# Kernel tuning notes

Hardware: AMD Instinct MI355X
Metric: run time of the kernel (lower is better)

## Reference

```python
import jax, jax.numpy as jnp
import numpy as np

B, S, D = 8, 2048, 256
H = 4
DH = D // H  # 64


def setup_inputs() -> dict:
    key = jax.random.key(0)
    ks = jax.random.split(key, 6)
    x = jax.random.normal(ks[0], (B, S, D), dtype=jnp.float32)
    # Linear weights stored as (d_in, d_out) so y = x @ W (+ b)
    scale = 1.0 / np.sqrt(D)
    w_q = jax.random.normal(ks[1], (D, D), dtype=jnp.float32) * scale
    w_k = jax.random.normal(ks[2], (D, D), dtype=jnp.float32) * scale
    w_v = jax.random.normal(ks[3], (D, D), dtype=jnp.float32) * scale
    w_o = jax.random.normal(ks[4], (D, D), dtype=jnp.float32) * scale
    b_o = jax.random.normal(ks[5], (D,), dtype=jnp.float32) * 0.01
    return {"x": x, "w_q": w_q, "w_k": w_k, "w_v": w_v, "w_o": w_o, "b_o": b_o}


def reference(x, w_q, w_k, w_v, w_o, b_o):
    b, s, _ = x.shape
    # project and split heads: [b, h, s, dh]
    q = (x @ w_q).reshape(b, s, H, DH).transpose(0, 2, 1, 3)
    k = (x @ w_k).reshape(b, s, H, DH).transpose(0, 2, 1, 3)
    v = (x @ w_v).reshape(b, s, H, DH).transpose(0, 2, 1, 3)
    # full attention matrix [b, h, s, s] (matches original non-fused math)
    scores = jnp.einsum('bhqd,bhkd->bhqk', q, k) / jnp.sqrt(jnp.float32(DH))
    attn = jax.nn.softmax(scores, axis=-1)  # dropout is identity in eval
    ctx = jnp.einsum('bhqk,bhkd->bhqd', attn, v)
    ctx = ctx.transpose(0, 2, 1, 3).reshape(b, s, H * DH)
    return ctx @ w_o + b_o
```

## Files before the change

kernel.cpp:

```cpp
#include <hip/hip_runtime.h>
#include <hip/hip_fp16.h>
#include <math.h>

typedef _Float16 f16;
typedef _Float16 f16x8 __attribute__((ext_vector_type(8)));
typedef float f32x4 __attribute__((ext_vector_type(4)));
typedef float f32x16 __attribute__((ext_vector_type(16)));
typedef unsigned int u32;
typedef unsigned int u32x4 __attribute__((ext_vector_type(4)));

#define BB 8
#define SS 2048
#define DD 256
#define HH 4
#define DHH 64

#define LOG2E 1.44269504088896340736f
#define MOFF2 (4.0f * LOG2E)
#define QSCALE (0.125f * LOG2E)

static __device__ __forceinline__ u32 pkrtz(float a, float b) {
  auto t = __builtin_amdgcn_cvt_pkrtz(a, b);
  return __builtin_bit_cast(u32, t);
}

__global__ __launch_bounds__(256) void prep_kernel(
    const float* __restrict__ wq, const float* __restrict__ wk,
    const float* __restrict__ wv, const float* __restrict__ wo,
    f16* __restrict__ wqkvT, f16* __restrict__ woT) {
  __shared__ f16 lds[64][72];
  int dout0 = blockIdx.x * 64;
  int k0 = blockIdx.y * 64;
  const float* src;
  f16* dst;
  int col0, drow;
  if (dout0 < 256)      { src = wq; dst = wqkvT; col0 = dout0;       drow = dout0; }
  else if (dout0 < 512) { src = wk; dst = wqkvT; col0 = dout0 - 256; drow = dout0; }
  else if (dout0 < 768) { src = wv; dst = wqkvT; col0 = dout0 - 512; drow = dout0; }
  else                  { src = wo; dst = woT;   col0 = dout0 - 768; drow = dout0 - 768; }

  int dl = threadIdx.x & 63, kl = threadIdx.x >> 6;
#pragma unroll
  for (int i = 0; i < 16; i++) {
    int kloc = i * 4 + kl;
    lds[kloc][dl] = (f16)src[(size_t)(k0 + kloc) * 256 + col0 + dl];
  }
  __syncthreads();
  int row_l = threadIdx.x >> 2, kq = threadIdx.x & 3;
  f16x8 v0, v1;
#pragma unroll
  for (int j = 0; j < 8; j++) v0[j] = lds[kq * 16 + j][row_l];
#pragma unroll
  for (int j = 0; j < 8; j++) v1[j] = lds[kq * 16 + 8 + j][row_l];
  f16* p = dst + (size_t)(drow + row_l) * 256 + k0 + kq * 16;
  *(f16x8*)p = v0;
  *(f16x8*)(p + 8) = v1;
}

__global__ __launch_bounds__(256) void qkv_gemm(
    const float* __restrict__ x, const f16* __restrict__ wT,
    f16* __restrict__ Q, f16* __restrict__ K, f16* __restrict__ VT) {
  __shared__ __attribute__((aligned(16))) f16 astage[8][4][64][8];
  __shared__ __attribute__((aligned(16))) f16 bstage[8][4][64][8];
  __shared__ __attribute__((aligned(16))) f16 lds_t[64][72];
  int m0 = blockIdx.x * 64;
  int wave = threadIdx.x >> 6, lane = threadIdx.x & 63;
  int lm = lane & 15, quad = lane >> 4;
  int bb = m0 >> 11, s0 = m0 & 2047;

  {
    int row = threadIdx.x >> 2;
    int c0 = (threadIdx.x & 3) * 64;
    const float* xr = x + (size_t)(m0 + row) * 256 + c0;
#pragma unroll
    for (int i = 0; i < 8; i++) {
      f32x4 lo = *(const f32x4*)(xr + i * 8);
      f32x4 hi = *(const f32x4*)(xr + i * 8 + 4);
      f16x8 v;
#pragma unroll
      for (int j = 0; j < 4; j++) { v[j] = (f16)lo[j]; v[j + 4] = (f16)hi[j]; }
      int col = c0 + i * 8;
      *(f16x8*)&astage[col >> 5][row >> 4][((col >> 3) & 3) * 16 + (row & 15)][0] = v;
    }
  }
  __syncthreads();
  f16x8 a[8];
#pragma unroll
  for (int kk = 0; kk < 8; kk++) a[kk] = *(const f16x8*)&astage[kk][wave][lane][0];

  f16x8 breg[8];
  auto bload = [&](int n0) {
#pragma unroll
    for (int kk = 0; kk < 8; kk++)
      breg[kk] = *(const f16x8*)(wT + (size_t)(n0 + wave * 16 + lm) * 256 + kk * 32 + quad * 8);
  };
  bload(0);

  for (int i = 0; i < 12; i++) {
#pragma unroll
    for (int kk = 0; kk < 8; kk++)
      *(f16x8*)&bstage[kk][wave][lane][0] = breg[kk];
    __syncthreads();
    if (i + 1 < 12) bload((i + 1) * 64);

    f32x4 acc[4] = {};
#pragma unroll
    for (int kk = 0; kk < 8; kk++)
#pragma unroll
      for (int nt = 0; nt < 4; nt++) {
        f16x8 b = *(const f16x8*)&bstage[kk][nt][lane][0];
        acc[nt] = __builtin_amdgcn_mfma_f32_16x16x32_f16(a[kk], b, acc[nt], 0, 0, 0);
      }

    int h = i & 3;
    if (i < 8) {
      float qsc = (i < 4) ? QSCALE : 1.0f;
#pragma unroll
      for (int nt = 0; nt < 4; nt++)
#pragma unroll
        for (int r = 0; r < 4; r++)
          lds_t[wave * 16 + quad * 4 + r][nt * 16 + lm] = (f16)(acc[nt][r] * qsc);
      __syncthreads();
      int rr = threadIdx.x >> 2, cc = threadIdx.x & 3;
      f16* dst = ((i < 4) ? Q : K) +
                 (((size_t)(bb * HH + h) * SS + s0 + rr) << 6) + cc * 16;
      *(f16x8*)dst = *(const f16x8*)&lds_t[rr][cc * 16];
      *(f16x8*)(dst + 8) = *(const f16x8*)&lds_t[rr][cc * 16 + 8];
    } else {
#pragma unroll
      for (int nt = 0; nt < 4; nt++)
#pragma unroll
        for (int r = 0; r < 4; r++)
          lds_t[nt * 16 + lm][wave * 16 + quad * 4 + r] = (f16)acc[nt][r];
      __syncthreads();
      int rr = threadIdx.x >> 2, cc = threadIdx.x & 3;
      f16* vrow = VT + ((size_t)(bb * HH + h) * DHH + rr) * SS + s0;
      *(f16x8*)(vrow + cc * 16) = *(const f16x8*)&lds_t[rr][cc * 16];
      *(f16x8*)(vrow + cc * 16 + 8) = *(const f16x8*)&lds_t[rr][cc * 16 + 8];
    }
    __syncthreads();
  }
}

__global__ __launch_bounds__(512, 2) void attn_kernel(
    const f16* __restrict__ Q, const f16* __restrict__ K,
    const f16* __restrict__ VT, f16* __restrict__ ctx) {
  __shared__ __attribute__((aligned(16))) f16 kv[2][2][2][8][64][8];

  int qb = blockIdx.x, hd = blockIdx.y, b = blockIdx.z;
  int w = threadIdx.x >> 6, lane = threadIdx.x & 63;
  int half = w >> 2, wl = w & 3;
  int l31 = lane & 31, hi = lane >> 5, hi8 = hi * 8;
  const f16* Qbh = Q + (size_t)(b * HH + hd) * SS * DHH;
  const f16* Kbh = K + (size_t)(b * HH + hd) * SS * DHH;
  const f16* Vbh = VT + (size_t)(b * HH + hd) * DHH * SS;
  int q0 = qb * 128 + wl * 32;
  int kh0 = half * 1024;

  f16x8 tk0, tk1, tv0, tv1;
  auto stage_load = [&](int key0) {
    tk0 = *(const f16x8*)(Kbh + (size_t)(key0 + l31) * DHH + wl * 16 + hi8);
    tk1 = *(const f16x8*)(Kbh + (size_t)(key0 + 32 + l31) * DHH + wl * 16 + hi8);
    tv0 = *(const f16x8*)(Vbh + (size_t)l31 * SS + key0 + wl * 16 + hi8);
    tv1 = *(const f16x8*)(Vbh + (size_t)(32 + l31) * SS + key0 + wl * 16 + hi8);
  };
  auto stage_write = [&](int buf) {
    *(f16x8*)&kv[half][buf][0][wl][lane][0] = tk0;
    *(f16x8*)&kv[half][buf][0][4 + wl][lane][0] = tk1;
    *(f16x8*)&kv[half][buf][1][wl][lane][0] = tv0;
    *(f16x8*)&kv[half][buf][1][4 + wl][lane][0] = tv1;
  };

  f16x8 aq[4];
  {
    const f16* qrow = Qbh + (size_t)(q0 + l31) * DHH + hi8;
#pragma unroll
    for (int kp = 0; kp < 4; kp++) aq[kp] = *(const f16x8*)(qrow + kp * 16);
  }
  f16x8 vones;
#pragma unroll
  for (int j = 0; j < 8; j++) vones[j] = (f16)1.0f;
  f32x16 minit;
#pragma unroll
  for (int r = 0; r < 16; r++) minit[r] = -MOFF2;

  f32x16 accO0, accO1, accL;
#pragma unroll
  for (int r = 0; r < 16; r++) { accO0[r] = 0.f; accO1[r] = 0.f; accL[r] = 0.f; }

  stage_load(kh0);
  stage_write(0);
  stage_load(kh0 + 64);

  const int NT = 1024 / 64;
  for (int t = 0; t < NT; t++) {
    int cur = t & 1;
    __syncthreads();

    if (t + 1 < NT) {
      stage_write(cur ^ 1);
      if (t + 2 < NT) stage_load(kh0 + (t + 2) * 64);
    }

    f32x16 accST[2];
#pragma unroll
    for (int kp = 0; kp < 4; kp++)
#pragma unroll
      for (int nt = 0; nt < 2; nt++) {
        f16x8 kf = *(const f16x8*)&kv[half][cur][0][nt * 4 + kp][lane][0];
        accST[nt] = __builtin_amdgcn_mfma_f32_32x32x16_f16(
            kf, aq[kp], kp == 0 ? minit : accST[nt], 0, 0, 0);
      }

    f16x8 pa[4];
#pragma unroll
    for (int nt = 0; nt < 2; nt++) {
      u32 u[4][2];
#pragma unroll
      for (int bq = 0; bq < 4; bq++) {
        float p0 = __builtin_amdgcn_exp2f(accST[nt][4 * bq + 0]);
        float p1 = __builtin_amdgcn_exp2f(accST[nt][4 * bq + 1]);
        float p2 = __builtin_amdgcn_exp2f(accST[nt][4 * bq + 2]);
        float p3 = __builtin_amdgcn_exp2f(accST[nt][4 * bq + 3]);
        u[bq][0] = pkrtz(p0, p1);
        u[bq][1] = pkrtz(p2, p3);
      }
#pragma unroll
      for (int sl = 0; sl < 2; sl++) {
        auto r0 = __builtin_amdgcn_permlane32_swap(u[2 * sl][0], u[2 * sl + 1][0],
                                                   false, false);
        auto r1 = __builtin_amdgcn_permlane32_swap(u[2 * sl][1], u[2 * sl + 1][1],
                                                   false, false);
        u32x4 wv = {(u32)r0[0], (u32)r1[0], (u32)r0[1], (u32)r1[1]};
        pa[nt * 2 + sl] = __builtin_bit_cast(f16x8, wv);
      }
    }

#pragma unroll
    for (int ks = 0; ks < 4; ks++) {
      accL = __builtin_amdgcn_mfma_f32_32x32x16_f16(pa[ks], vones, accL, 0, 0, 0);
      f16x8 v0 = *(const f16x8*)&kv[half][cur][1][ks][lane][0];
      accO0 = __builtin_amdgcn_mfma_f32_32x32x16_f16(pa[ks], v0, accO0, 0, 0, 0);
      f16x8 v1 = *(const f16x8*)&kv[half][cur][1][4 + ks][lane][0];
      accO1 = __builtin_amdgcn_mfma_f32_32x32x16_f16(pa[ks], v1, accO1, 0, 0, 0);
    }
  }

  __syncthreads();
  float* scratch = (float*)kv;
  int sbase = (wl * 64 + lane) * 49;
  if (half == 1) {
#pragma unroll
    for (int r = 0; r < 16; r++) {
      scratch[sbase + r]      = accO0[r];
      scratch[sbase + 16 + r] = accO1[r];
      scratch[sbase + 32 + r] = accL[r];
    }
  }
  __syncthreads();
  if (half == 0) {
#pragma unroll
    for (int r = 0; r < 16; r++) {
      float o0 = accO0[r] + scratch[sbase + r];
      float o1 = accO1[r] + scratch[sbase + 16 + r];
      float rinv = __builtin_amdgcn_rcpf(accL[r] + scratch[sbase + 32 + r]);
      int s = q0 + (r & 3) + 8 * (r >> 2) + 4 * hi;
      f16* dst = ctx + (size_t)(b * SS + s) * DD + hd * DHH + l31;
      dst[0]  = (f16)(o0 * rinv);
      dst[32] = (f16)(o1 * rinv);
    }
  }
}

__global__ __launch_bounds__(256) void out_gemm(
    const f16* __restrict__ ctxh, const f16* __restrict__ woT,
    const float* __restrict__ bo, float* __restrict__ out) {
  __shared__ __attribute__((aligned(16))) f16 astage[8][4][64][8];
  __shared__ __attribute__((aligned(16))) f16 bstage[8][4][64][8];
  int m0 = blockIdx.x * 64;
  int wave = threadIdx.x >> 6, lane = threadIdx.x & 63;
  int lm = lane & 15, quad = lane >> 4;

  {
    int row = threadIdx.x >> 2;
    int c0 = (threadIdx.x & 3) * 64;
    const f16* cr = ctxh + (size_t)(m0 + row) * 256 + c0;
#pragma unroll
    for (int i = 0; i < 8; i++) {
      f16x8 v = *(const f16x8*)(cr + i * 8);
      int col = c0 + i * 8;
      *(f16x8*)&astage[col >> 5][row >> 4][((col >> 3) & 3) * 16 + (row & 15)][0] = v;
    }
  }
  __syncthreads();
  f16x8 a[8];
#pragma unroll
  for (int kk = 0; kk < 8; kk++) a[kk] = *(const f16x8*)&astage[kk][wave][lane][0];

  f16x8 breg[8];
  auto bload = [&](int n0) {
#pragma unroll
    for (int kk = 0; kk < 8; kk++)
      breg[kk] = *(const f16x8*)(woT + (size_t)(n0 + wave * 16 + lm) * 256 + kk * 32 + quad * 8);
  };
  bload(0);

  for (int i = 0; i < 4; i++) {
    int n0 = i * 64;
#pragma unroll
    for (int kk = 0; kk < 8; kk++)
      *(f16x8*)&bstage[kk][wave][lane][0] = breg[kk];
    __syncthreads();
    if (i + 1 < 4) bload((i + 1) * 64);

    f32x4 acc[4] = {};
#pragma unroll
    for (int kk = 0; kk < 8; kk++)
#pragma unroll
      for (int nt = 0; nt < 4; nt++) {
        f16x8 bfr = *(const f16x8*)&bstage[kk][nt][lane][0];
        acc[nt] = __builtin_amdgcn_mfma_f32_16x16x32_f16(a[kk], bfr, acc[nt], 0, 0, 0);
      }
#pragma unroll
    for (int nt = 0; nt < 4; nt++) {
      int dout = n0 + nt * 16 + lm;
      float bias = bo[dout];
#pragma unroll
      for (int r = 0; r < 4; r++) {
        int t = m0 + wave * 16 + quad * 4 + r;
        out[(size_t)t * 256 + dout] = acc[nt][r] + bias;
      }
    }
    __syncthreads();
  }
}

extern "C" void kernel_launch(void* const* d_in, const int* in_sizes, int n_in,
                              void* d_out, int out_size, void* d_ws, size_t ws_size,
                              hipStream_t stream) {
  const float* x  = (const float*)d_in[0];
  const float* wq = (const float*)d_in[1];
  const float* wk = (const float*)d_in[2];
  const float* wv = (const float*)d_in[3];
  const float* wo = (const float*)d_in[4];
  const float* bo = (const float*)d_in[5];
  float* out = (float*)d_out;

  char* ws = (char*)d_ws;
  const size_t SZ = 8388608;
  f16* Qb    = (f16*)(ws);
  f16* Kb    = (f16*)(ws + SZ);
  f16* VTb   = (f16*)(ws + 2 * SZ);
  f16* ctxh  = (f16*)(ws + 3 * SZ);
  f16* wqkvT = (f16*)(ws + 4 * SZ);
  f16* woT   = (f16*)(ws + 4 * SZ + 393216);

  hipLaunchKernelGGL(prep_kernel, dim3(16, 4), dim3(256), 0, stream,
                     wq, wk, wv, wo, wqkvT, woT);
  hipLaunchKernelGGL(qkv_gemm, dim3(256), dim3(256), 0, stream,
                     x, wqkvT, Qb, Kb, VTb);
  hipLaunchKernelGGL(attn_kernel, dim3(16, 4, 8), dim3(512), 0, stream,
                     Qb, Kb, VTb, ctxh);
  hipLaunchKernelGGL(out_gemm, dim3(256), dim3(256), 0, stream,
                     ctxh, woT, bo, out);
}
```

Before: 156.3 us.

## Split attention key halves into separate blocks and merge partials in output GEMM

Each key half of the attention now runs as its own 256-thread block rather than as half of a 512-thread block. Every block writes its unnormalized fp16 context and row sums to separate global buffers, and the output GEMM adds the two partials and normalizes while staging its A tile. This removes the in-block LDS reduction and its two barriers, doubles the number of blocks available for scheduling, and allows more resident blocks per CU. In exchange it adds a second context buffer plus a row-sum buffer, extra global reads and writes, and rounds the unnormalized partial sums to fp16, which costs some precision.

```diff
diff --git a/kernel.cpp b/kernel.cpp
--- a/kernel.cpp
+++ b/kernel.cpp
@@ -142,33 +142,35 @@
   }
 }
 
-__global__ __launch_bounds__(512, 2) void attn_kernel(
+__global__ __launch_bounds__(256, 4) void attn_kernel(
     const f16* __restrict__ Q, const f16* __restrict__ K,
-    const f16* __restrict__ VT, f16* __restrict__ ctx) {
-  __shared__ __attribute__((aligned(16))) f16 kv[2][2][2][8][64][8];
-
-  int qb = blockIdx.x, hd = blockIdx.y, b = blockIdx.z;
+    const f16* __restrict__ VT, f16* __restrict__ ctx0,
+    f16* __restrict__ ctx1, float* __restrict__ lsum) {
+  __shared__ __attribute__((aligned(16))) f16 kbuf[2][8][64][8];
+  __shared__ __attribute__((aligned(16))) f16 vbuf[2][8][64][8];
+
+  int half = blockIdx.x & 1, qb = blockIdx.x >> 1;
+  int hd = blockIdx.y, b = blockIdx.z;
   int w = threadIdx.x >> 6, lane = threadIdx.x & 63;
-  int half = w >> 2, wl = w & 3;
   int l31 = lane & 31, hi = lane >> 5, hi8 = hi * 8;
   const f16* Qbh = Q + (size_t)(b * HH + hd) * SS * DHH;
   const f16* Kbh = K + (size_t)(b * HH + hd) * SS * DHH;
   const f16* Vbh = VT + (size_t)(b * HH + hd) * DHH * SS;
-  int q0 = qb * 128 + wl * 32;
+  int q0 = qb * 128 + w * 32;
   int kh0 = half * 1024;
 
   f16x8 tk0, tk1, tv0, tv1;
   auto stage_load = [&](int key0) {
-    tk0 = *(const f16x8*)(Kbh + (size_t)(key0 + l31) * DHH + wl * 16 + hi8);
-    tk1 = *(const f16x8*)(Kbh + (size_t)(key0 + 32 + l31) * DHH + wl * 16 + hi8);
-    tv0 = *(const f16x8*)(Vbh + (size_t)l31 * SS + key0 + wl * 16 + hi8);
-    tv1 = *(const f16x8*)(Vbh + (size_t)(32 + l31) * SS + key0 + wl * 16 + hi8);
+    tk0 = *(const f16x8*)(Kbh + (size_t)(key0 + l31) * DHH + w * 16 + hi8);
+    tk1 = *(const f16x8*)(Kbh + (size_t)(key0 + 32 + l31) * DHH + w * 16 + hi8);
+    tv0 = *(const f16x8*)(Vbh + (size_t)l31 * SS + key0 + w * 16 + hi8);
+    tv1 = *(const f16x8*)(Vbh + (size_t)(32 + l31) * SS + key0 + w * 16 + hi8);
   };
   auto stage_write = [&](int buf) {
-    *(f16x8*)&kv[half][buf][0][wl][lane][0] = tk0;
-    *(f16x8*)&kv[half][buf][0][4 + wl][lane][0] = tk1;
-    *(f16x8*)&kv[half][buf][1][wl][lane][0] = tv0;
-    *(f16x8*)&kv[half][buf][1][4 + wl][lane][0] = tv1;
+    *(f16x8*)&kbuf[buf][w][lane][0] = tk0;
+    *(f16x8*)&kbuf[buf][4 + w][lane][0] = tk1;
+    *(f16x8*)&vbuf[buf][w][lane][0] = tv0;
+    *(f16x8*)&vbuf[buf][4 + w][lane][0] = tv1;
   };
 
   f16x8 aq[4];
@@ -207,7 +209,7 @@
     for (int kp = 0; kp < 4; kp++)
 #pragma unroll
       for (int nt = 0; nt < 2; nt++) {
-        f16x8 kf = *(const f16x8*)&kv[half][cur][0][nt * 4 + kp][lane][0];
+        f16x8 kf = *(const f16x8*)&kbuf[cur][nt * 4 + kp][lane][0];
         accST[nt] = __builtin_amdgcn_mfma_f32_32x32x16_f16(
             kf, aq[kp], kp == 0 ? minit : accST[nt], 0, 0, 0);
       }
@@ -239,41 +241,32 @@
 #pragma unroll
     for (int ks = 0; ks < 4; ks++) {
       accL = __builtin_amdgcn_mfma_f32_32x32x16_f16(pa[ks], vones, accL, 0, 0, 0);
-      f16x8 v0 = *(const f16x8*)&kv[half][cur][1][ks][lane][0];
+      f16x8 v0 = *(const f16x8*)&vbuf[cur][ks][lane][0];
       accO0 = __builtin_amdgcn_mfma_f32_32x32x16_f16(pa[ks], v0, accO0, 0, 0, 0);
-      f16x8 v1 = *(const f16x8*)&kv[half][cur][1][4 + ks][lane][0];
+      f16x8 v1 = *(const f16x8*)&vbuf[cur][4 + ks][lane][0];
       accO1 = __builtin_amdgcn_mfma_f32_32x32x16_f16(pa[ks], v1, accO1, 0, 0, 0);
     }
   }
 
-  __syncthreads();
-  float* scratch = (float*)kv;
-  int sbase = (wl * 64 + lane) * 49;
-  if (half == 1) {
-#pragma unroll
-    for (int r = 0; r < 16; r++) {
-      scratch[sbase + r]      = accO0[r];
-      scratch[sbase + 16 + r] = accO1[r];
-      scratch[sbase + 32 + r] = accL[r];
-    }
-  }
-  __syncthreads();
-  if (half == 0) {
-#pragma unroll
-    for (int r = 0; r < 16; r++) {
-      float o0 = accO0[r] + scratch[sbase + r];
-      float o1 = accO1[r] + scratch[sbase + 16 + r];
-      float rinv = __builtin_amdgcn_rcpf(accL[r] + scratch[sbase + 32 + r]);
-      int s = q0 + (r & 3) + 8 * (r >> 2) + 4 * hi;
-      f16* dst = ctx + (size_t)(b * SS + s) * DD + hd * DHH + l31;
-      dst[0]  = (f16)(o0 * rinv);
-      dst[32] = (f16)(o1 * rinv);
-    }
+  f16* ctxp = half ? ctx1 : ctx0;
+#pragma unroll
+  for (int r = 0; r < 16; r++) {
+    int s = q0 + (r & 3) + 8 * (r >> 2) + 4 * hi;
+    f16* dst = ctxp + (size_t)(b * SS + s) * DD + hd * DHH + l31;
+    dst[0]  = (f16)accO0[r];
+    dst[32] = (f16)accO1[r];
+  }
+  if (l31 == 0) {
+    float* lp = lsum + (size_t)half * (BB * HH * SS) + (size_t)(b * HH + hd) * SS;
+#pragma unroll
+    for (int r = 0; r < 16; r++)
+      lp[q0 + (r & 3) + 8 * (r >> 2) + 4 * hi] = accL[r];
   }
 }
 
 __global__ __launch_bounds__(256) void out_gemm(
-    const f16* __restrict__ ctxh, const f16* __restrict__ woT,
+    const f16* __restrict__ ctx0, const f16* __restrict__ ctx1,
+    const float* __restrict__ lsum, const f16* __restrict__ woT,
     const float* __restrict__ bo, float* __restrict__ out) {
   __shared__ __attribute__((aligned(16))) f16 astage[8][4][64][8];
   __shared__ __attribute__((aligned(16))) f16 bstage[8][4][64][8];
@@ -284,10 +277,22 @@
   {
     int row = threadIdx.x >> 2;
     int c0 = (threadIdx.x & 3) * 64;
-    const f16* cr = ctxh + (size_t)(m0 + row) * 256 + c0;
+    int h = threadIdx.x & 3;
+    int t = m0 + row;
+    int bb = t >> 11, ss = t & 2047;
+    size_t lidx = (size_t)(bb * HH + h) * SS + ss;
+    float l = lsum[lidx] + lsum[(size_t)(BB * HH * SS) + lidx];
+    float rinv = __builtin_amdgcn_rcpf(l);
+    const f16* p0 = ctx0 + (size_t)t * 256 + c0;
+    const f16* p1 = ctx1 + (size_t)t * 256 + c0;
 #pragma unroll
     for (int i = 0; i < 8; i++) {
-      f16x8 v = *(const f16x8*)(cr + i * 8);
+      f16x8 v0 = *(const f16x8*)(p0 + i * 8);
+      f16x8 v1 = *(const f16x8*)(p1 + i * 8);
+      f16x8 v;
+#pragma unroll
+      for (int j = 0; j < 8; j++)
+        v[j] = (f16)(((float)v0[j] + (float)v1[j]) * rinv);
       int col = c0 + i * 8;
       *(f16x8*)&astage[col >> 5][row >> 4][((col >> 3) & 3) * 16 + (row & 15)][0] = v;
     }
@@ -351,16 +356,18 @@
   f16* Qb    = (f16*)(ws);
   f16* Kb    = (f16*)(ws + SZ);
   f16* VTb   = (f16*)(ws + 2 * SZ);
-  f16* ctxh  = (f16*)(ws + 3 * SZ);
-  f16* wqkvT = (f16*)(ws + 4 * SZ);
-  f16* woT   = (f16*)(ws + 4 * SZ + 393216);
+  f16* ctx0  = (f16*)(ws + 3 * SZ);
+  f16* ctx1  = (f16*)(ws + 4 * SZ);
+  f16* wqkvT = (f16*)(ws + 5 * SZ);
+  f16* woT   = (f16*)(ws + 5 * SZ + 393216);
+  float* lsum = (float*)(ws + 5 * SZ + 393216 + 131072);
 
   hipLaunchKernelGGL(prep_kernel, dim3(16, 4), dim3(256), 0, stream,
                      wq, wk, wv, wo, wqkvT, woT);
   hipLaunchKernelGGL(qkv_gemm, dim3(256), dim3(256), 0, stream,
                      x, wqkvT, Qb, Kb, VTb);
-  hipLaunchKernelGGL(attn_kernel, dim3(16, 4, 8), dim3(512), 0, stream,
-                     Qb, Kb, VTb, ctxh);
+  hipLaunchKernelGGL(attn_kernel, dim3(32, 4, 8), dim3(256), 0, stream,
+                     Qb, Kb, VTb, ctx0, ctx1, lsum);
   hipLaunchKernelGGL(out_gemm, dim3(256), dim3(256), 0, stream,
-                     ctxh, woT, bo, out);
-}
+                     ctx0, ctx1, lsum, woT, bo, out);
+}
```

Measured after the change: 263.4 us. 68.6% more time.

## Fuse all stages into one persistent kernel with atomic grid barriers

Applied to the files above, without the earlier changes.

Replaces the four separate launches (weight prep, QKV GEMM, attention, output GEMM) with a single persistent kernel of 512 blocks that separates stages using atomic-counter grid barriers. The QKV and output GEMMs are split across two blocks per row tile, and attention is restructured so each 256-thread block walks all keys instead of splitting keys across two half-blocks and merging through LDS. The aim is to remove launch gaps and tail effects between stages. In exchange it depends on all blocks being co-resident to avoid deadlock, and it halves the waves available to the attention stage while lengthening each wave's key loop.

```diff
diff --git a/kernel.cpp b/kernel.cpp
--- a/kernel.cpp
+++ b/kernel.cpp
@@ -24,314 +24,313 @@
   return __builtin_bit_cast(u32, t);
 }
 
-__global__ __launch_bounds__(256) void prep_kernel(
-    const float* __restrict__ wq, const float* __restrict__ wk,
-    const float* __restrict__ wv, const float* __restrict__ wo,
-    f16* __restrict__ wqkvT, f16* __restrict__ woT) {
-  __shared__ f16 lds[64][72];
-  int dout0 = blockIdx.x * 64;
-  int k0 = blockIdx.y * 64;
-  const float* src;
-  f16* dst;
-  int col0, drow;
-  if (dout0 < 256)      { src = wq; dst = wqkvT; col0 = dout0;       drow = dout0; }
-  else if (dout0 < 512) { src = wk; dst = wqkvT; col0 = dout0 - 256; drow = dout0; }
-  else if (dout0 < 768) { src = wv; dst = wqkvT; col0 = dout0 - 512; drow = dout0; }
-  else                  { src = wo; dst = woT;   col0 = dout0 - 768; drow = dout0 - 768; }
-
-  int dl = threadIdx.x & 63, kl = threadIdx.x >> 6;
-#pragma unroll
-  for (int i = 0; i < 16; i++) {
-    int kloc = i * 4 + kl;
-    lds[kloc][dl] = (f16)src[(size_t)(k0 + kloc) * 256 + col0 + dl];
-  }
+static __device__ __forceinline__ void gsync(unsigned* cnt, unsigned target) {
+  __threadfence();
   __syncthreads();
-  int row_l = threadIdx.x >> 2, kq = threadIdx.x & 3;
-  f16x8 v0, v1;
-#pragma unroll
-  for (int j = 0; j < 8; j++) v0[j] = lds[kq * 16 + j][row_l];
-#pragma unroll
-  for (int j = 0; j < 8; j++) v1[j] = lds[kq * 16 + 8 + j][row_l];
-  f16* p = dst + (size_t)(drow + row_l) * 256 + k0 + kq * 16;
-  *(f16x8*)p = v0;
-  *(f16x8*)(p + 8) = v1;
+  if (threadIdx.x == 0) {
+    atomicAdd(cnt, 1u);
+    while (atomicAdd(cnt, 0u) < target) __builtin_amdgcn_s_sleep(8);
+  }
+  __syncthreads();
+  __threadfence();
 }
 
-__global__ __launch_bounds__(256) void qkv_gemm(
-    const float* __restrict__ x, const f16* __restrict__ wT,
-    f16* __restrict__ Q, f16* __restrict__ K, f16* __restrict__ VT) {
-  __shared__ __attribute__((aligned(16))) f16 astage[8][4][64][8];
-  __shared__ __attribute__((aligned(16))) f16 bstage[8][4][64][8];
-  __shared__ __attribute__((aligned(16))) f16 lds_t[64][72];
-  int m0 = blockIdx.x * 64;
+__global__ __launch_bounds__(256) void fused_kernel(
+    const float* __restrict__ x, const float* __restrict__ wq,
+    const float* __restrict__ wk, const float* __restrict__ wv,
+    const float* __restrict__ wo, const float* __restrict__ bo,
+    f16* __restrict__ wqkvT, f16* __restrict__ woT,
+    f16* __restrict__ Q, f16* __restrict__ K, f16* __restrict__ VT,
+    f16* __restrict__ ctx, float* __restrict__ out, unsigned* cnt) {
+  __shared__ __attribute__((aligned(16))) char smem[65536];
+  int bid = blockIdx.x;
   int wave = threadIdx.x >> 6, lane = threadIdx.x & 63;
   int lm = lane & 15, quad = lane >> 4;
-  int bb = m0 >> 11, s0 = m0 & 2047;
+  const unsigned NB = gridDim.x;
+
+  if (bid < 64) {
+    f16 (*lds)[72] = (f16(*)[72])smem;
+    int dout0 = (bid & 15) * 64;
+    int k0 = (bid >> 4) * 64;
+    const float* src;
+    f16* dst;
+    int col0, drow;
+    if (dout0 < 256)      { src = wq; dst = wqkvT; col0 = dout0;       drow = dout0; }
+    else if (dout0 < 512) { src = wk; dst = wqkvT; col0 = dout0 - 256; drow = dout0; }
+    else if (dout0 < 768) { src = wv; dst = wqkvT; col0 = dout0 - 512; drow = dout0; }
+    else                  { src = wo; dst = woT;   col0 = dout0 - 768; drow = dout0 - 768; }
+
+    int dl = threadIdx.x & 63, kl = threadIdx.x >> 6;
+#pragma unroll
+    for (int i = 0; i < 16; i++) {
+      int kloc = i * 4 + kl;
+      lds[kloc][dl] = (f16)src[(size_t)(k0 + kloc) * 256 + col0 + dl];
+    }
+    __syncthreads();
+    int row_l = threadIdx.x >> 2, kq = threadIdx.x & 3;
+    f16x8 v0, v1;
+#pragma unroll
+    for (int j = 0; j < 8; j++) v0[j] = lds[kq * 16 + j][row_l];
+#pragma unroll
+    for (int j = 0; j < 8; j++) v1[j] = lds[kq * 16 + 8 + j][row_l];
+    f16* p = dst + (size_t)(drow + row_l) * 256 + k0 + kq * 16;
+    *(f16x8*)p = v0;
+    *(f16x8*)(p + 8) = v1;
+  }
+  gsync(&cnt[0], NB);
 
   {
-    int row = threadIdx.x >> 2;
-    int c0 = (threadIdx.x & 3) * 64;
-    const float* xr = x + (size_t)(m0 + row) * 256 + c0;
-#pragma unroll
-    for (int i = 0; i < 8; i++) {
-      f32x4 lo = *(const f32x4*)(xr + i * 8);
-      f32x4 hi = *(const f32x4*)(xr + i * 8 + 4);
-      f16x8 v;
-#pragma unroll
-      for (int j = 0; j < 4; j++) { v[j] = (f16)lo[j]; v[j + 4] = (f16)hi[j]; }
-      int col = c0 + i * 8;
-      *(f16x8*)&astage[col >> 5][row >> 4][((col >> 3) & 3) * 16 + (row & 15)][0] = v;
-    }
-  }
-  __syncthreads();
-  f16x8 a[8];
-#pragma unroll
-  for (int kk = 0; kk < 8; kk++) a[kk] = *(const f16x8*)&astage[kk][wave][lane][0];
-
-  f16x8 breg[8];
-  auto bload = [&](int n0) {
-#pragma unroll
-    for (int kk = 0; kk < 8; kk++)
-      breg[kk] = *(const f16x8*)(wT + (size_t)(n0 + wave * 16 + lm) * 256 + kk * 32 + quad * 8);
-  };
-  bload(0);
-
-  for (int i = 0; i < 12; i++) {
-#pragma unroll
-    for (int kk = 0; kk < 8; kk++)
-      *(f16x8*)&bstage[kk][wave][lane][0] = breg[kk];
+    f16 (*astage)[4][64][8] = (f16(*)[4][64][8])smem;
+    f16 (*bstage)[4][64][8] = (f16(*)[4][64][8])(smem + 32768);
+    f16 (*lds_t)[72] = (f16(*)[72])smem;
+    int m0 = (bid >> 1) * 64;
+    int i0 = (bid & 1) * 6, iend = i0 + 6;
+    int bb = m0 >> 11, s0 = m0 & 2047;
+
+    {
+      int row = threadIdx.x >> 2;
+      int c0 = (threadIdx.x & 3) * 64;
+      const float* xr = x + (size_t)(m0 + row) * 256 + c0;
+#pragma unroll
+      for (int i = 0; i < 8; i++) {
+        f32x4 lo = *(const f32x4*)(xr + i * 8);
+        f32x4 hh = *(const f32x4*)(xr + i * 8 + 4);
+        f16x8 v;
+#pragma unroll
+        for (int j = 0; j < 4; j++) { v[j] = (f16)lo[j]; v[j + 4] = (f16)hh[j]; }
+        int col = c0 + i * 8;
+        *(f16x8*)&astage[col >> 5][row >> 4][((col >> 3) & 3) * 16 + (row & 15)][0] = v;
+      }
+    }
     __syncthreads();
-    if (i + 1 < 12) bload((i + 1) * 64);
-
-    f32x4 acc[4] = {};
-#pragma unroll
-    for (int kk = 0; kk < 8; kk++)
-#pragma unroll
-      for (int nt = 0; nt < 4; nt++) {
-        f16x8 b = *(const f16x8*)&bstage[kk][nt][lane][0];
-        acc[nt] = __builtin_amdgcn_mfma_f32_16x16x32_f16(a[kk], b, acc[nt], 0, 0, 0);
-      }
-
-    int h = i & 3;
-    if (i < 8) {
-      float qsc = (i < 4) ? QSCALE : 1.0f;
-#pragma unroll
-      for (int nt = 0; nt < 4; nt++)
-#pragma unroll
-        for (int r = 0; r < 4; r++)
-          lds_t[wave * 16 + quad * 4 + r][nt * 16 + lm] = (f16)(acc[nt][r] * qsc);
-      __syncthreads();
-      int rr = threadIdx.x >> 2, cc = threadIdx.x & 3;
-      f16* dst = ((i < 4) ? Q : K) +
-                 (((size_t)(bb * HH + h) * SS + s0 + rr) << 6) + cc * 16;
-      *(f16x8*)dst = *(const f16x8*)&lds_t[rr][cc * 16];
-      *(f16x8*)(dst + 8) = *(const f16x8*)&lds_t[rr][cc * 16 + 8];
-    } else {
-#pragma unroll
-      for (int nt = 0; nt < 4; nt++)
-#pragma unroll
-        for (int r = 0; r < 4; r++)
-          lds_t[nt * 16 + lm][wave * 16 + quad * 4 + r] = (f16)acc[nt][r];
-      __syncthreads();
-      int rr = threadIdx.x >> 2, cc = threadIdx.x & 3;
-      f16* vrow = VT + ((size_t)(bb * HH + h) * DHH + rr) * SS + s0;
-      *(f16x8*)(vrow + cc * 16) = *(const f16x8*)&lds_t[rr][cc * 16];
-      *(f16x8*)(vrow + cc * 16 + 8) = *(const f16x8*)&lds_t[rr][cc * 16 + 8];
-    }
-    __syncthreads();
-  }
-}
-
-__global__ __launch_bounds__(512, 2) void attn_kernel(
-    const f16* __restrict__ Q, const f16* __restrict__ K,
-    const f16* __restrict__ VT, f16* __restrict__ ctx) {
-  __shared__ __attribute__((aligned(16))) f16 kv[2][2][2][8][64][8];
-
-  int qb = blockIdx.x, hd = blockIdx.y, b = blockIdx.z;
-  int w = threadIdx.x >> 6, lane = threadIdx.x & 63;
-  int half = w >> 2, wl = w & 3;
-  int l31 = lane & 31, hi = lane >> 5, hi8 = hi * 8;
-  const f16* Qbh = Q + (size_t)(b * HH + hd) * SS * DHH;
-  const f16* Kbh = K + (size_t)(b * HH + hd) * SS * DHH;
-  const f16* Vbh = VT + (size_t)(b * HH + hd) * DHH * SS;
-  int q0 = qb * 128 + wl * 32;
-  int kh0 = half * 1024;
-
-  f16x8 tk0, tk1, tv0, tv1;
-  auto stage_load = [&](int key0) {
-    tk0 = *(const f16x8*)(Kbh + (size_t)(key0 + l31) * DHH + wl * 16 + hi8);
-    tk1 = *(const f16x8*)(Kbh + (size_t)(key0 + 32 + l31) * DHH + wl * 16 + hi8);
-    tv0 = *(const f16x8*)(Vbh + (size_t)l31 * SS + key0 + wl * 16 + hi8);
-    tv1 = *(const f16x8*)(Vbh + (size_t)(32 + l31) * SS + key0 + wl * 16 + hi8);
-  };
-  auto stage_write = [&](int buf) {
-    *(f16x8*)&kv[half][buf][0][wl][lane][0] = tk0;
-    *(f16x8*)&kv[half][buf][0][4 + wl][lane][0] = tk1;
-    *(f16x8*)&kv[half][buf][1][wl][lane][0] = tv0;
-    *(f16x8*)&kv[half][buf][1][4 + wl][lane][0] = tv1;
-  };
-
-  f16x8 aq[4];
+    f16x8 a[8];
+#pragma unroll
+    for (int kk = 0; kk < 8; kk++) a[kk] = *(const f16x8*)&astage[kk][wave][lane][0];
+
+    f16x8 breg[8];
+    auto bload = [&](int n0) {
+#pragma unroll
+      for (int kk = 0; kk < 8; kk++)
+        breg[kk] = *(const f16x8*)(wqkvT + (size_t)(n0 + wave * 16 + lm) * 256 + kk * 32 + quad * 8);
+    };
+    bload(i0 * 64);
+
+    for (int i = i0; i < iend; i++) {
+#pragma unroll
+      for (int kk = 0; kk < 8; kk++)
+        *(f16x8*)&bstage[kk][wave][lane][0] = breg[kk];
+      __syncthreads();
+      if (i + 1 < iend) bload((i + 1) * 64);
+
+      f32x4 acc[4] = {};
+#pragma unroll
+      for (int kk = 0; kk < 8; kk++)
+#pragma unroll
+        for (int nt = 0; nt < 4; nt++) {
+          f16x8 b = *(const f16x8*)&bstage[kk][nt][lane][0];
+          acc[nt] = __builtin_amdgcn_mfma_f32_16x16x32_f16(a[kk], b, acc[nt], 0, 0, 0);
+        }
+
+      int h = i & 3;
+      if (i < 8) {
+        float qsc = (i < 4) ? QSCALE : 1.0f;
+#pragma unroll
+        for (int nt = 0; nt < 4; nt++)
+#pragma unroll
+          for (int r = 0; r < 4; r++)
+            lds_t[wave * 16 + quad * 4 + r][nt * 16 + lm] = (f16)(acc[nt][r] * qsc);
+        __syncthreads();
+        int rr = threadIdx.x >> 2, cc = threadIdx.x & 3;
+        f16* dst = ((i < 4) ? Q : K) +
+                   (((size_t)(bb * HH + h) * SS + s0 + rr) << 6) + cc * 16;
+        *(f16x8*)dst = *(const f16x8*)&lds_t[rr][cc * 16];
+        *(f16x8*)(dst + 8) = *(const f16x8*)&lds_t[rr][cc * 16 + 8];
+      } else {
+#pragma unroll
+        for (int nt = 0; nt < 4; nt++)
+#pragma unroll
+          for (int r = 0; r < 4; r++)
+            lds_t[nt * 16 + lm][wave * 16 + quad * 4 + r] = (f16)acc[nt][r];
+        __syncthreads();
+        int rr = threadIdx.x >> 2, cc = threadIdx.x & 3;
+        f16* vrow = VT + ((size_t)(bb * HH + h) * DHH + rr) * SS + s0;
+        *(f16x8*)(vrow + cc * 16) = *(const f16x8*)&lds_t[rr][cc * 16];
+        *(f16x8*)(vrow + cc * 16 + 8) = *(const f16x8*)&lds_t[rr][cc * 16 + 8];
+      }
+      __syncthreads();
+    }
+  }
+  gsync(&cnt[1], NB);
+
   {
-    const f16* qrow = Qbh + (size_t)(q0 + l31) * DHH + hi8;
-#pragma unroll
-    for (int kp = 0; kp < 4; kp++) aq[kp] = *(const f16x8*)(qrow + kp * 16);
-  }
-  f16x8 vones;
-#pragma unroll
-  for (int j = 0; j < 8; j++) vones[j] = (f16)1.0f;
-  f32x16 minit;
-#pragma unroll
-  for (int r = 0; r < 16; r++) minit[r] = -MOFF2;
-
-  f32x16 accO0, accO1, accL;
-#pragma unroll
-  for (int r = 0; r < 16; r++) { accO0[r] = 0.f; accO1[r] = 0.f; accL[r] = 0.f; }
-
-  stage_load(kh0);
-  stage_write(0);
-  stage_load(kh0 + 64);
-
-  const int NT = 1024 / 64;
-  for (int t = 0; t < NT; t++) {
-    int cur = t & 1;
-    __syncthreads();
-
-    if (t + 1 < NT) {
-      stage_write(cur ^ 1);
-      if (t + 2 < NT) stage_load(kh0 + (t + 2) * 64);
-    }
-
-    f32x16 accST[2];
-#pragma unroll
-    for (int kp = 0; kp < 4; kp++)
+    f16 (*kbuf)[8][64][8] = (f16(*)[8][64][8])smem;
+    f16 (*vbuf)[8][64][8] = (f16(*)[8][64][8])(smem + 16384);
+    int qb = bid & 15, hd = (bid >> 4) & 3, b = bid >> 6;
+    int w = wave;
+    int l31 = lane & 31, hi = lane >> 5, hi8 = hi * 8;
+    const f16* Qbh = Q + (size_t)(b * HH + hd) * SS * DHH;
+    const f16* Kbh = K + (size_t)(b * HH + hd) * SS * DHH;
+    const f16* Vbh = VT + (size_t)(b * HH + hd) * DHH * SS;
+    int q0 = qb * 128 + w * 32;
+
+    f16x8 tk0, tk1, tv0, tv1;
+    auto stage_load = [&](int key0) {
+      tk0 = *(const f16x8*)(Kbh + (size_t)(key0 + l31) * DHH + w * 16 + hi8);
+      tk1 = *(const f16x8*)(Kbh + (size_t)(key0 + 32 + l31) * DHH + w * 16 + hi8);
+      tv0 = *(const f16x8*)(Vbh + (size_t)l31 * SS + key0 + w * 16 + hi8);
+      tv1 = *(const f16x8*)(Vbh + (size_t)(32 + l31) * SS + key0 + w * 16 + hi8);
+    };
+    auto stage_write = [&](int buf) {
+      *(f16x8*)&kbuf[buf][w][lane][0] = tk0;
+      *(f16x8*)&kbuf[buf][4 + w][lane][0] = tk1;
+      *(f16x8*)&vbuf[buf][w][lane][0] = tv0;
+      *(f16x8*)&vbuf[buf][4 + w][lane][0] = tv1;
+    };
+
+    f16x8 aq[4];
+    {
+      const f16* qrow = Qbh + (size_t)(q0 + l31) * DHH + hi8;
+#pragma unroll
+      for (int kp = 0; kp < 4; kp++) aq[kp] = *(const f16x8*)(qrow + kp * 16);
+    }
+    f16x8 vones;
+#pragma unroll
+    for (int j = 0; j < 8; j++) vones[j] = (f16)1.0f;
+    f32x16 minit;
+#pragma unroll
+    for (int r = 0; r < 16; r++) minit[r] = -MOFF2;
+
+    f32x16 accO0, accO1, accL;
+#pragma unroll
+    for (int r = 0; r < 16; r++) { accO0[r] = 0.f; accO1[r] = 0.f; accL[r] = 0.f; }
+
+    stage_load(0);
+    stage_write(0);
+    stage_load(64);
+
+    const int NT = SS / 64;
+    for (int t = 0; t < NT; t++) {
+      int cur = t & 1;
+      __syncthreads();
+
+      if (t + 1 < NT) {
+        stage_write(cur ^ 1);
+        if (t + 2 < NT) stage_load((t + 2) * 64);
+      }
+
+      f32x16 accST[2];
+#pragma unroll
+      for (int kp = 0; kp < 4; kp++)
+#pragma unroll
+        for (int nt = 0; nt < 2; nt++) {
+          f16x8 kf = *(const f16x8*)&kbuf[cur][nt * 4 + kp][lane][0];
+          accST[nt] = __builtin_amdgcn_mfma_f32_32x32x16_f16(
+              kf, aq[kp], kp == 0 ? minit : accST[nt], 0, 0, 0);
+        }
+
+      f16x8 pa[4];
 #pragma unroll
       for (int nt = 0; nt < 2; nt++) {
-        f16x8 kf = *(const f16x8*)&kv[half][cur][0][nt * 4 + kp][lane][0];
-        accST[nt] = __builtin_amdgcn_mfma_f32_32x32x16_f16(
-            kf, aq[kp], kp == 0 ? minit : accST[nt], 0, 0, 0);
-      }
-
-    f16x8 pa[4];
-#pragma unroll
-    for (int nt = 0; nt < 2; nt++) {
-      u32 u[4][2];
-#pragma unroll
-      for (int bq = 0; bq < 4; bq++) {
-        float p0 = __builtin_amdgcn_exp2f(accST[nt][4 * bq + 0]);
-        float p1 = __builtin_amdgcn_exp2f(accST[nt][4 * bq + 1]);
-        float p2 = __builtin_amdgcn_exp2f(accST[nt][4 * bq + 2]);
-        float p3 = __builtin_amdgcn_exp2f(accST[nt][4 * bq + 3]);
-        u[bq][0] = pkrtz(p0, p1);
-        u[bq][1] = pkrtz(p2, p3);
-      }
-#pragma unroll
-      for (int sl = 0; sl < 2; sl++) {
-        auto r0 = __builtin_amdgcn_permlane32_swap(u[2 * sl][0], u[2 * sl + 1][0],
-                                                   false, false);
-        auto r1 = __builtin_amdgcn_permlane32_swap(u[2 * sl][1], u[2 * sl + 1][1],
-                                                   false, false);
-        u32x4 wv = {(u32)r0[0], (u32)r1[0], (u32)r0[1], (u32)r1[1]};
-        pa[nt * 2 + sl] = __builtin_bit_cast(f16x8, wv);
-      }
-    }
-
-#pragma unroll
-    for (int ks = 0; ks < 4; ks++) {
-      accL = __builtin_amdgcn_mfma_f32_32x32x16_f16(pa[ks], vones, accL, 0, 0, 0);
-      f16x8 v0 = *(const f16x8*)&kv[half][cur][1][ks][lane][0];
-      accO0 = __builtin_amdgcn_mfma_f32_32x32x16_f16(pa[ks], v0, accO0, 0, 0, 0);
-      f16x8 v1 = *(const f16x8*)&kv[half][cur][1][4 + ks][lane][0];
-      accO1 = __builtin_amdgcn_mfma_f32_32x32x16_f16(pa[ks], v1, accO1, 0, 0, 0);
-    }
-  }
-
-  __syncthreads();
-  float* scratch = (float*)kv;
-  int sbase = (wl * 64 + lane) * 49;
-  if (half == 1) {
+        u32 u[4][2];
+#pragma unroll
+        for (int bq = 0; bq < 4; bq++) {
+          float p0 = __builtin_amdgcn_exp2f(accST[nt][4 * bq + 0]);
+          float p1 = __builtin_amdgcn_exp2f(accST[nt][4 * bq + 1]);
+          float p2 = __builtin_amdgcn_exp2f(accST[nt][4 * bq + 2]);
+          float p3 = __builtin_amdgcn_exp2f(accST[nt][4 * bq + 3]);
+          u[bq][0] = pkrtz(p0, p1);
+          u[bq][1] = pkrtz(p2, p3);
+        }
+#pragma unroll
+        for (int sl = 0; sl < 2; sl++) {
+          auto r0 = __builtin_amdgcn_permlane32_swap(u[2 * sl][0], u[2 * sl + 1][0],
+                                                     false, false);
+          auto r1 = __builtin_amdgcn_permlane32_swap(u[2 * sl][1], u[2 * sl + 1][1],
+                                                     false, false);
+          u32x4 wv = {(u32)r0[0], (u32)r1[0], (u32)r0[1], (u32)r1[1]};
+          pa[nt * 2 + sl] = __builtin_bit_cast(f16x8, wv);
+        }
+      }
+
+#pragma unroll
+      for (int ks = 0; ks < 4; ks++) {
+        accL = __builtin_amdgcn_mfma_f32_32x32x16_f16(pa[ks], vones, accL, 0, 0, 0);
+        f16x8 v0 = *(const f16x8*)&vbuf[cur][ks][lane][0];
+        accO0 = __builtin_amdgcn_mfma_f32_32x32x16_f16(pa[ks], v0, accO0, 0, 0, 0);
+        f16x8 v1 = *(const f16x8*)&vbuf[cur][4 + ks][lane][0];
+        accO1 = __builtin_amdgcn_mfma_f32_32x32x16_f16(pa[ks], v1, accO1, 0, 0, 0);
+      }
+    }
+
 #pragma unroll
     for (int r = 0; r < 16; r++) {
-      scratch[sbase + r]      = accO0[r];
-      scratch[sbase + 16 + r] = accO1[r];
-      scratch[sbase + 32 + r] = accL[r];
-    }
-  }
-  __syncthreads();
-  if (half == 0) {
-#pragma unroll
-    for (int r = 0; r < 16; r++) {
-      float o0 = accO0[r] + scratch[sbase + r];
-      float o1 = accO1[r] + scratch[sbase + 16 + r];
-      float rinv = __builtin_amdgcn_rcpf(accL[r] + scratch[sbase + 32 + r]);
+      float rinv = __builtin_amdgcn_rcpf(accL[r]);
       int s = q0 + (r & 3) + 8 * (r >> 2) + 4 * hi;
       f16* dst = ctx + (size_t)(b * SS + s) * DD + hd * DHH + l31;
-      dst[0]  = (f16)(o0 * rinv);
-      dst[32] = (f16)(o1 * rinv);
-    }
-  }
-}
-
-__global__ __launch_bounds__(256) void out_gemm(
-    const f16* __restrict__ ctxh, const f16* __restrict__ woT,
-    const float* __restrict__ bo, float* __restrict__ out) {
-  __shared__ __attribute__((aligned(16))) f16 astage[8][4][64][8];
-  __shared__ __attribute__((aligned(16))) f16 bstage[8][4][64][8];
-  int m0 = blockIdx.x * 64;
-  int wave = threadIdx.x >> 6, lane = threadIdx.x & 63;
-  int lm = lane & 15, quad = lane >> 4;
+      dst[0]  = (f16)(accO0[r] * rinv);
+      dst[32] = (f16)(accO1[r] * rinv);
+    }
+  }
+  gsync(&cnt[2], NB);
 
   {
-    int row = threadIdx.x >> 2;
-    int c0 = (threadIdx.x & 3) * 64;
-    const f16* cr = ctxh + (size_t)(m0 + row) * 256 + c0;
-#pragma unroll
-    for (int i = 0; i < 8; i++) {
-      f16x8 v = *(const f16x8*)(cr + i * 8);
-      int col = c0 + i * 8;
-      *(f16x8*)&astage[col >> 5][row >> 4][((col >> 3) & 3) * 16 + (row & 15)][0] = v;
-    }
-  }
-  __syncthreads();
-  f16x8 a[8];
-#pragma unroll
-  for (int kk = 0; kk < 8; kk++) a[kk] = *(const f16x8*)&astage[kk][wave][lane][0];
-
-  f16x8 breg[8];
-  auto bload = [&](int n0) {
-#pragma unroll
-    for (int kk = 0; kk < 8; kk++)
-      breg[kk] = *(const f16x8*)(woT + (size_t)(n0 + wave * 16 + lm) * 256 + kk * 32 + quad * 8);
-  };
-  bload(0);
-
-  for (int i = 0; i < 4; i++) {
-    int n0 = i * 64;
-#pragma unroll
-    for (int kk = 0; kk < 8; kk++)
-      *(f16x8*)&bstage[kk][wave][lane][0] = breg[kk];
+    f16 (*astage)[4][64][8] = (f16(*)[4][64][8])smem;
+    f16 (*bstage)[4][64][8] = (f16(*)[4][64][8])(smem + 32768);
+    int m0 = (bid >> 1) * 64;
+    int nh = bid & 1;
+
+    {
+      int row = threadIdx.x >> 2;
+      int c0 = (threadIdx.x & 3) * 64;
+      const f16* cr = ctx + (size_t)(m0 + row) * 256 + c0;
+#pragma unroll
+      for (int i = 0; i < 8; i++) {
+        f16x8 v = *(const f16x8*)(cr + i * 8);
+        int col = c0 + i * 8;
+        *(f16x8*)&astage[col >> 5][row >> 4][((col >> 3) & 3) * 16 + (row & 15)][0] = v;
+      }
+    }
     __syncthreads();
-    if (i + 1 < 4) bload((i + 1) * 64);
-
-    f32x4 acc[4] = {};
-#pragma unroll
-    for (int kk = 0; kk < 8; kk++)
+    f16x8 a[8];
+#pragma unroll
+    for (int kk = 0; kk < 8; kk++) a[kk] = *(const f16x8*)&astage[kk][wave][lane][0];
+
+    f16x8 breg[8];
+    auto bload = [&](int n0) {
+#pragma unroll
+      for (int kk = 0; kk < 8; kk++)
+        breg[kk] = *(const f16x8*)(woT + (size_t)(n0 + wave * 16 + lm) * 256 + kk * 32 + quad * 8);
+    };
+    bload(nh * 128);
+
+    for (int i = 0; i < 2; i++) {
+      int n0 = nh * 128 + i * 64;
+#pragma unroll
+      for (int kk = 0; kk < 8; kk++)
+        *(f16x8*)&bstage[kk][wave][lane][0] = breg[kk];
+      __syncthreads();
+      if (i + 1 < 2) bload(nh * 128 + 64);
+
+      f32x4 acc[4] = {};
+#pragma unroll
+      for (int kk = 0; kk < 8; kk++)
+#pragma unroll
+        for (int nt = 0; nt < 4; nt++) {
+          f16x8 bfr = *(const f16x8*)&bstage[kk][nt][lane][0];
+          acc[nt] = __builtin_amdgcn_mfma_f32_16x16x32_f16(a[kk], bfr, acc[nt], 0, 0, 0);
+        }
 #pragma unroll
       for (int nt = 0; nt < 4; nt++) {
-        f16x8 bfr = *(const f16x8*)&bstage[kk][nt][lane][0];
-        acc[nt] = __builtin_amdgcn_mfma_f32_16x16x32_f16(a[kk], bfr, acc[nt], 0, 0, 0);
-      }
-#pragma unroll
-    for (int nt = 0; nt < 4; nt++) {
-      int dout = n0 + nt * 16 + lm;
-      float bias = bo[dout];
-#pragma unroll
-      for (int r = 0; r < 4; r++) {
-        int t = m0 + wave * 16 + quad * 4 + r;
-        out[(size_t)t * 256 + dout] = acc[nt][r] + bias;
-      }
-    }
-    __syncthreads();
+        int dout = n0 + nt * 16 + lm;
+        float bias = bo[dout];
+#pragma unroll
+        for (int r = 0; r < 4; r++) {
+          int t = m0 + wave * 16 + quad * 4 + r;
+          out[(size_t)t * 256 + dout] = acc[nt][r] + bias;
+        }
+      }
+      __syncthreads();
+    }
   }
 }
 
@@ -354,13 +353,10 @@
   f16* ctxh  = (f16*)(ws + 3 * SZ);
   f16* wqkvT = (f16*)(ws + 4 * SZ);
   f16* woT   = (f16*)(ws + 4 * SZ + 393216);
-
-  hipLaunchKernelGGL(prep_kernel, dim3(16, 4), dim3(256), 0, stream,
-                     wq, wk, wv, wo, wqkvT, woT);
-  hipLaunchKernelGGL(qkv_gemm, dim3(256), dim3(256), 0, stream,
-                     x, wqkvT, Qb, Kb, VTb);
-  hipLaunchKernelGGL(attn_kernel, dim3(16, 4, 8), dim3(512), 0, stream,
-                     Qb, Kb, VTb, ctxh);
-  hipLaunchKernelGGL(out_gemm, dim3(256), dim3(256), 0, stream,
-                     ctxh, woT, bo, out);
+  unsigned* cnt = (unsigned*)(ws + 4 * SZ + 393216 + 131072);
+
+  hipMemsetAsync(cnt, 0, 3 * sizeof(unsigned), stream);
+  hipLaunchKernelGGL(fused_kernel, dim3(512), dim3(256), 0, stream,
+                     x, wq, wk, wv, wo, bo, wqkvT, woT, Qb, Kb, VTb, ctxh,
+                     out, cnt);
 }
```

Result: slower. 495.4 us (+217.0%).
